# Kernel tuning notes

Hardware: AMD Instinct MI355X
Metric: run time of the kernel (lower is better)

## Reference

```python
import jax, jax.numpy as jnp
import numpy as np

# promonet-derived constants
S = 64        # FARGAN_SUBFRAME_SIZE
NSUB = 4      # FARGAN_SUBFRAMES
HOP = 256     # HOPSIZE = S * NSUB
L = 512       # HOPSIZE * FARGAN_PREVIOUS_FRAMES
F = 193       # acoustic features (192) + pitch period channel
G = 64        # GLOBAL_CHANNELS
CH = F - 1 + G  # conditioning width = 256
B = 64
FRAMES = 100


def setup_inputs() -> dict:
    key = jax.random.key(0)
    ks = jax.random.split(key, 24)

    def w(k, o, i):
        return jax.random.normal(k, (o, i), jnp.float32) / np.sqrt(i).astype(np.float32)

    feat = jax.random.normal(ks[0], (B, F - 1, FRAMES), jnp.float32)
    # last channel is the pitch period (rounded to int inside the model)
    period = jax.random.randint(ks[1], (B, 1, FRAMES), 64, 300).astype(jnp.float32)
    features = jnp.concatenate([feat, period], axis=1)  # (B, F, FRAMES)
    return {
        "features": features,
        "global_features": jax.random.normal(ks[2], (B, G), jnp.float32),
        "previous_samples": 0.1 * jax.random.normal(ks[3], (B, L), jnp.float32),
        # conditioning network (3 bias-free linears, tanh after each)
        "Wc1": w(ks[4], CH, CH),
        "Wc2": w(ks[5], CH, CH),
        "Wc3": w(ks[6], 2 * HOP, CH),
        # framewise conv: linear over [subframe_input(4S+4), prev feat state(2S)]
        "Wfw": w(ks[7], S, 6 * S + 4),
        "Wfw_g": w(ks[8], S, S),
        # three GRU cells (bias-free), torch gate order r,z,n
        "Wih1": w(ks[9], 3 * S, 2 * S), "Whh1": w(ks[10], 3 * S, S),
        "Wih2": w(ks[11], 3 * S, 2 * S), "Whh2": w(ks[12], 3 * S, S),
        "Wih3": w(ks[13], 3 * S, 2 * S), "Whh3": w(ks[14], 3 * S, S),
        # GLU gates
        "Wg1": w(ks[15], S, S), "Wg2": w(ks[16], S, S), "Wg3": w(ks[17], S, S),
        "Wsg": w(ks[18], 2 * S, 2 * S),
        # skip dense + output
        "Wsd": w(ks[19], 2 * S, 5 * S),
        "Wout": w(ks[20], S, 2 * S),
    }


def _glu(x, Wg):
    return x * jax.nn.sigmoid(x @ Wg.T)


def _gru(x, h, Wih, Whh):
    gi = x @ Wih.T
    gh = h @ Whh.T
    ir, iz, inew = jnp.split(gi, 3, axis=-1)
    hr, hz, hnew = jnp.split(gh, 3, axis=-1)
    r = jax.nn.sigmoid(ir + hr)
    z = jax.nn.sigmoid(iz + hz)
    n = jnp.tanh(inew + r * hnew)
    return (1.0 - z) * n + z * h


def reference(features, global_features, previous_samples,
              Wc1, Wc2, Wc3, Wfw, Wfw_g,
              Wih1, Whh1, Wih2, Whh2, Wih3, Whh3,
              Wg1, Wg2, Wg3, Wsg, Wsd, Wout):
    Bn = features.shape[0]
    lb_ar = jnp.arange(S + 4)

    def subframe(feat2s, prev, period, states):
        s1, s2, s3, sfw = states
        prev_sub = prev[:, -S:]
        # data-dependent pitch lookback gather with wrap for short periods
        idx = L - period[:, None] + lb_ar[None, :] - 2
        idx = idx - period[:, None] * (idx >= L)
        lookback = jnp.take_along_axis(prev, idx, axis=1)  # (B, S+4)
        sub_in = jnp.concatenate([feat2s, prev_sub, lookback], axis=1)  # (B, 4S+4)
        fw = _glu(jnp.tanh(jnp.concatenate([sub_in, sfw], axis=1) @ Wfw.T), Wfw_g)
        g1 = _gru(jnp.concatenate([fw, prev_sub], 1), s1, Wih1, Whh1)
        o1 = _glu(g1, Wg1)
        g2 = _gru(jnp.concatenate([o1, prev_sub], 1), s2, Wih2, Whh2)
        o2 = _glu(g2, Wg2)
        g3 = _gru(jnp.concatenate([o2, prev_sub], 1), s3, Wih3, Whh3)
        o3 = _glu(g3, Wg3)
        skip = jnp.concatenate([o1, o2, o3, fw, prev_sub], 1)  # (B, 5S)
        so = _glu(jnp.tanh(skip @ Wsd.T), Wsg)
        out = jnp.tanh(so @ Wout.T)  # (B, S)
        return out, (g1, g2, g3, feat2s)

    def frame_step(carry, feat_t):
        prev, states = carry
        period = jnp.round(feat_t[:, -1]).astype(jnp.int32)
        x = jnp.concatenate([feat_t[:, :-1], global_features], axis=1)
        c = jnp.tanh(jnp.tanh(jnp.tanh(x @ Wc1.T) @ Wc2.T) @ Wc3.T)  # (B, 2*HOP)
        subs = c.reshape(Bn, 2 * S, NSUB)
        outs = []
        for k in range(NSUB):  # fixed tiny unroll over subframes
            out, states = subframe(subs[:, :, k], prev, period, states)
            prev = jnp.concatenate([prev[:, S:], out], axis=1)
            outs.append(out)
        return (prev, states), jnp.concatenate(outs, axis=1)  # (B, HOP)

    dt = features.dtype
    states0 = (jnp.zeros((Bn, S), dt), jnp.zeros((Bn, S), dt),
               jnp.zeros((Bn, S), dt), jnp.zeros((Bn, 2 * S), dt))
    feats_t = jnp.transpose(features, (2, 0, 1))  # (frames, B, F)
    _, sigs = jax.lax.scan(frame_step, (previous_samples, states0), feats_t)
    # (frames, B, HOP) -> (B, 1, frames*HOP)
    return jnp.transpose(sigs, (1, 0, 2)).reshape(Bn, 1, -1)
```

## Files before the change

kernel.cpp:

```cpp
#include <hip/hip_runtime.h>
#include <hip/hip_bf16.h>

#define SS      64
#define NSUB    4
#define LPREV   512
#define NF      193
#define NFRAMES 100
#define BATCH   64
#define RPW     16

typedef __attribute__((ext_vector_type(8))) short   short8;
typedef __attribute__((ext_vector_type(4))) float   floatx4;

__device__ __forceinline__ float bf2f(unsigned short u) {
    return __uint_as_float(((unsigned int)u) << 16);
}
__device__ __forceinline__ unsigned short f2bf(float x) {
    unsigned int u = __float_as_uint(x);
    return (unsigned short)((u + 0x7fffu + ((u >> 16) & 1u)) >> 16);
}
__device__ __forceinline__ unsigned int packbf(float a, float b) {
    return (unsigned int)f2bf(a) | ((unsigned int)f2bf(b) << 16);
}
__device__ __forceinline__ float fexp2(float x) {
#if __has_builtin(__builtin_amdgcn_exp2f)
    return __builtin_amdgcn_exp2f(x);
#else
    return exp2f(x);
#endif
}
__device__ __forceinline__ float frcp(float x) {
#if __has_builtin(__builtin_amdgcn_rcpf)
    return __builtin_amdgcn_rcpf(x);
#else
    return 1.0f / x;
#endif
}
__device__ __forceinline__ float fsig(float x) {
    return frcp(1.0f + fexp2(-1.442695041f * x));
}
__device__ __forceinline__ float ftanh(float x) {
    return fmaf(2.0f, frcp(1.0f + fexp2(-2.885390082f * x)), -1.0f);
}
__device__ __forceinline__ float ld1f(int f32, const void* p, size_t i) {
    if (f32) return ((const float*)p)[i];
    return bf2f(((const unsigned short*)p)[i]);
}
__device__ __forceinline__ float lo16(unsigned int u) { return __uint_as_float(u << 16); }
__device__ __forceinline__ float hi16(unsigned int u) { return __uint_as_float(u & 0xffff0000u); }

__device__ __forceinline__ floatx4 mf(short8 a, short8 b, floatx4 c) {
    return __builtin_amdgcn_mfma_f32_16x16x32_bf16(a, b, c, 0, 0, 0);
}

__device__ __forceinline__ short8 ldA(const unsigned short* buf, int strideU,
                                      int m, int kb, int q) {
    const unsigned int* p = (const unsigned int*)buf + m * strideU + kb * 16 + q * 4;
    uint4 u = *(const uint4*)p;
    return __builtin_bit_cast(short8, u);
}
__device__ __forceinline__ short8 ldB(const uint4* __restrict__ w, int idx) {
    return __builtin_bit_cast(short8, w[idx]);
}

#define OFF_FW   0
#define OFF_FWG  3328
#define OFF_GRU(G) (3840 + 4608*(G))
#define OFF_WG(G)  (17664 + 512*(G))
#define OFF_SD   19200
#define OFF_SG   24320
#define OFF_OUT  26368
#define NFRAG    27392

__global__ void fargan_detect(const void* feats, int* flag) {
    const float* pf = (const float*)feats;
    int ok = 1;
    for (int f = 0; f < 50; ++f) {
        float v = pf[192 * NFRAMES + f];
        if (!(v >= 63.0f && v <= 301.0f)) { ok = 0; break; }
    }
    *flag = ok;
}

__global__ __launch_bounds__(256) void fargan_prep(
    const int* __restrict__ flag,
    const void* Wfw, const void* Wfwg,
    const void* Wih1, const void* Whh1, const void* Wih2, const void* Whh2,
    const void* Wih3, const void* Whh3,
    const void* Wg1, const void* Wg2, const void* Wg3,
    const void* Wsg, const void* Wsd, const void* Wout,
    uint4* __restrict__ wbuf)
{
    int fi = blockIdx.x * 256 + threadIdx.x;
    if (fi >= NFRAG) return;
    int f32 = *flag;
    const void* mats[14] = {Wfw, Wfwg, Wih1, Whh1, Wih2, Whh2, Wih3, Whh3,
                            Wg1, Wg2, Wg3, Wsg, Wsd, Wout};
    const int NSEG = 20;
    const int sb[NSEG]  = {0,3328, 3840,5376,6912,7936, 8448,9984,11520,12544,
                           13056,14592,16128,17152, 17664,18176,18688, 19200,24320,26368};
    const int sa[NSEG]  = {0,1, 2,2,2,3, 4,4,4,5, 6,6,6,7, 8,9,10, 12,11,13};
    const int sbx[NSEG] = {-1,-1, 3,3,-1,-1, 5,5,-1,-1, 7,7,-1,-1, -1,-1,-1, -1,-1,-1};
    const int sro[NSEG] = {0,0, 0,64,128,128, 0,64,128,128, 0,64,128,128, 0,0,0, 0,0,0};
    const int skb[NSEG] = {13,2, 6,6,4,2, 6,6,4,2, 6,6,4,2, 2,2,2, 10,4,4};
    const int ska[NSEG] = {388,64, 128,128,128,64, 128,128,128,64, 128,128,128,64,
                           64,64,64, 320,128,128};
    const int skr[NSEG] = {388,64, 192,192,128,64, 192,192,128,64, 192,192,128,64,
                           64,64,64, 320,128,128};
    int s = 0;
    for (int i = 1; i < NSEG; ++i) if (fi >= sb[i]) s = i;
    int local = fi - sb[s];
    int ln = local & 15, lq = (local >> 4) & 3, tkb = local >> 6;
    int KB = skb[s];
    int kb = tkb % KB, tile = tkb / KB;
    int row = sro[s] + tile * 16 + ln;
    int Ka = ska[s], Kr = skr[s];
    union { unsigned short h[8]; uint4 v; } u;
#pragma unroll
    for (int j = 0; j < 8; ++j) {
        int k = kb * 32 + lq * 8 + j;
        unsigned short val = 0;
        if (k < Kr) {
            const void* m; size_t off;
            if (sbx[s] >= 0 && k >= Ka) { m = mats[sbx[s]]; off = (size_t)row * 64 + (k - Ka); }
            else                        { m = mats[sa[s]];  off = (size_t)row * Ka + k; }
            val = f32 ? f2bf(((const float*)m)[off]) : ((const unsigned short*)m)[off];
        }
        u.h[j] = val;
    }
    wbuf[fi] = u.v;
}

__global__ __launch_bounds__(256) void fargan_prep_conv(
    const int* __restrict__ flag,
    const void* Wc1, const void* Wc2, const void* Wc3,
    unsigned int* __restrict__ wct)
{
    int idx = blockIdx.x * 256 + threadIdx.x;
    if (idx >= 131072) return;
    int f32 = *flag;
    const void* W; int n, k2;
    if (idx < 32768)      { W = Wc1; k2 = idx >> 8, n = idx & 255; }
    else if (idx < 65536) { W = Wc2; k2 = (idx - 32768) >> 8; n = idx & 255; }
    else                  { W = Wc3; k2 = (idx - 65536) >> 9; n = (idx - 65536) & 511; }
    size_t off = (size_t)n * 256 + 2 * k2;
    unsigned int v;
    if (f32) {
        const float* p = (const float*)W + off;
        v = packbf(p[0], p[1]);
    } else {
        v = *(const unsigned int*)((const unsigned short*)W + off);
    }
    wct[idx] = v;
}

template<bool F32>
__device__ __forceinline__ void conv_body(
    const void* __restrict__ feats, const void* __restrict__ gfeat,
    const unsigned int* __restrict__ wct, float* __restrict__ cbuf)
{
    int blk = blockIdx.x;
    int b = blk / NFRAMES, f = blk - b * NFRAMES;
    int t = threadIdx.x;
    __shared__ float xa[256], xb[256];

    float v;
    if (t < 192) v = ld1f(F32 ? 1 : 0, feats, (size_t)b * (NF * NFRAMES) + t * NFRAMES + f);
    else         v = ld1f(F32 ? 1 : 0, gfeat, (size_t)b * 64 + (t - 192));
    xa[t] = v;
    __syncthreads();

    const unsigned int* w1 = wct;
    const unsigned int* w2 = wct + 32768;
    const unsigned int* w3 = wct + 65536;

    float a0 = 0.f, a1 = 0.f;
#pragma unroll 8
    for (int k2 = 0; k2 < 128; ++k2) {
        unsigned int u = w1[k2 * 256 + t];
        a0 = fmaf(lo16(u), xa[2 * k2], a0);
        a1 = fmaf(hi16(u), xa[2 * k2 + 1], a1);
    }
    xb[t] = ftanh(a0 + a1);
    __syncthreads();

    a0 = 0.f; a1 = 0.f;
#pragma unroll 8
    for (int k2 = 0; k2 < 128; ++k2) {
        unsigned int u = w2[k2 * 256 + t];
        a0 = fmaf(lo16(u), xb[2 * k2], a0);
        a1 = fmaf(hi16(u), xb[2 * k2 + 1], a1);
    }
    xa[t] = ftanh(a0 + a1);
    __syncthreads();

    a0 = 0.f; a1 = 0.f;
    float b0 = 0.f, b1 = 0.f;
#pragma unroll 8
    for (int k2 = 0; k2 < 128; ++k2) {
        unsigned int u = w3[k2 * 512 + t];
        unsigned int u2 = w3[k2 * 512 + t + 256];
        a0 = fmaf(lo16(u),  xa[2 * k2],     a0);
        a1 = fmaf(hi16(u),  xa[2 * k2 + 1], a1);
        b0 = fmaf(lo16(u2), xa[2 * k2],     b0);
        b1 = fmaf(hi16(u2), xa[2 * k2 + 1], b1);
    }
    float* co = cbuf + ((size_t)b * NFRAMES + f) * 512;
    int e0 = t, e1 = t + 256;
    co[(e0 & 3) * 128 + (e0 >> 2)] = ftanh(a0 + a1);
    co[(e1 & 3) * 128 + (e1 >> 2)] = ftanh(b0 + b1);
}

__global__ __launch_bounds__(256) void fargan_conv(
    const void* feats, const void* gfeat,
    const int* flag, const unsigned int* wct, float* cbuf)
{
    if (*flag) conv_body<true>(feats, gfeat, wct, cbuf);
    else       conv_body<false>(feats, gfeat, wct, cbuf);
}


__global__ __launch_bounds__(256, 1) void fargan_seq(
    const void* __restrict__ feats, const void* __restrict__ prev_in,
    const int* __restrict__ flag, const float* __restrict__ cbuf,
    const uint4* __restrict__ wbuf, void* __restrict__ outp)
{
    const int t = threadIdx.x;
    const int b0 = blockIdx.x * RPW;
    const int lane = t & 63, w = t >> 6;
    const int lq = lane >> 4, ln = lane & 15;
    const int nj = 16 * w + ln;
    const int f32 = *flag;

    __shared__ __align__(16) unsigned short hist[RPW * 520];
    __shared__ __align__(16) unsigned short catb[RPW * 424];
    __shared__ __align__(16) unsigned short xg  [RPW * 200];
    __shared__ __align__(16) unsigned short skx [RPW * 328];
    __shared__ __align__(16) unsigned short sdbb[RPW * 136];
    __shared__ __align__(16) unsigned short sobb[RPW * 136];
    __shared__ __align__(16) unsigned short vpre[RPW * 72];
    __shared__ __align__(16) unsigned short svp [RPW * 72];
    __shared__ __align__(16) unsigned short wsd[128 * 328];
    __shared__ int period_s[RPW];

    short8 Bfw[13], Bfwg[2], Bout[4];
    short8 Br[3][6], Bz[3][6], Bi[3][4], Bh[3][2], Bg[3][2];
    short8 Bsg[2][4];
#pragma unroll
    for (int kb = 0; kb < 13; ++kb) Bfw[kb] = ldB(wbuf, OFF_FW + (w * 13 + kb) * 64 + lane);
#pragma unroll
    for (int kb = 0; kb < 2; ++kb)  Bfwg[kb] = ldB(wbuf, OFF_FWG + (w * 2 + kb) * 64 + lane);
#pragma unroll
    for (int G = 0; G < 3; ++G) {
        const int OR = OFF_GRU(G), OZ = OR + 1536, OI = OR + 3072, OH = OR + 4096;
#pragma unroll
        for (int kb = 0; kb < 6; ++kb) {
            Br[G][kb] = ldB(wbuf, OR + (w * 6 + kb) * 64 + lane);
            Bz[G][kb] = ldB(wbuf, OZ + (w * 6 + kb) * 64 + lane);
        }
#pragma unroll
        for (int kb = 0; kb < 4; ++kb) Bi[G][kb] = ldB(wbuf, OI + (w * 4 + kb) * 64 + lane);
#pragma unroll
        for (int kb = 0; kb < 2; ++kb) {
            Bh[G][kb] = ldB(wbuf, OH + (w * 2 + kb) * 64 + lane);
            Bg[G][kb] = ldB(wbuf, OFF_WG(G) + (w * 2 + kb) * 64 + lane);
        }
    }
#pragma unroll
    for (int tile = 0; tile < 2; ++tile)
#pragma unroll
        for (int kb = 0; kb < 4; ++kb)
            Bsg[tile][kb] = ldB(wbuf, OFF_SG + ((2 * w + tile) * 4 + kb) * 64 + lane);
#pragma unroll
    for (int kb = 0; kb < 4; ++kb) Bout[kb] = ldB(wbuf, OFF_OUT + (w * 4 + kb) * 64 + lane);

    for (int fi = t; fi < 8 * 10 * 64; fi += 256) {
        int lane2 = fi & 63, tkb = fi >> 6;
        int kb = tkb % 10, tile = tkb / 10;
        int lq2 = lane2 >> 4, ln2 = lane2 & 15;
        int row = tile * 16 + ln2;
        uint4 v = wbuf[OFF_SD + fi];
        *(uint4*)((unsigned int*)wsd + row * 164 + kb * 16 + lq2 * 4) = v;
    }

    for (int i = t; i < RPW * 424; i += 256) catb[i] = 0;
    for (int i = t; i < RPW * 200; i += 256) xg[i] = 0;
    for (int i = t; i < RPW * 328; i += 256) skx[i] = 0;
    for (int i = t; i < RPW * 136; i += 256) { sdbb[i] = 0; sobb[i] = 0; }
    for (int i = t; i < RPW * 72;  i += 256) { vpre[i] = 0; svp[i] = 0; }
    for (int i = t; i < RPW * 512; i += 256) {
        int row = i >> 9, c = i & 511;
        hist[row * 520 + c] = f2bf(ld1f(f32, prev_in, (size_t)(b0 + row) * LPREV + c));
    }
    __syncthreads();
    for (int i = t; i < RPW * 64; i += 256) {
        int row = i >> 6, c = i & 63;
        unsigned short h = hist[row * 520 + 448 + c];
        catb[row * 424 + 128 + c] = h;
        skx [row * 328 + 256 + c] = h;
        xg  [row * 200 + 64  + c] = h;
    }

    floatx4 svr[3];
#pragma unroll
    for (int G = 0; G < 3; ++G) svr[G] = (floatx4){0.f, 0.f, 0.f, 0.f};

    const int prow = t >> 4, px16 = t & 15, pe8 = (t & 15) * 8;
    float pfc[8];
    {
        const float* cr0 = cbuf + ((size_t)(b0 + prow) * NFRAMES + 0) * 512 + 0 * 128 + pe8;
#pragma unroll
        for (int i = 0; i < 8; ++i) pfc[i] = cr0[i];
    }
    float pper = 0.f;
    if (t < RPW)
        pper = ld1f(f32, feats, (size_t)(b0 + t) * (NF * NFRAMES) + (NF - 1) * NFRAMES + 0);
    __syncthreads();

    const floatx4 z4 = {0.f, 0.f, 0.f, 0.f};
    int base = 0;
    for (int f = 0; f < NFRAMES; ++f) {
        if (t < RPW) period_s[t] = (int)rintf(pper);
        __syncthreads();
        if (t < RPW) {
            int fN = (f + 1 < NFRAMES) ? f + 1 : f;
            pper = ld1f(f32, feats, (size_t)(b0 + t) * (NF * NFRAMES) + (NF - 1) * NFRAMES + fN);
        }

        for (int kk = 0; kk < NSUB; ++kk) {
            {
                int row = prow;
                unsigned int* cat32 = (unsigned int*)catb;
                int cb = row * 212;
                int e8 = pe8;
                unsigned int o0 = cat32[cb + (e8 >> 1) + 0];
                unsigned int o1 = cat32[cb + (e8 >> 1) + 1];
                unsigned int o2 = cat32[cb + (e8 >> 1) + 2];
                unsigned int o3 = cat32[cb + (e8 >> 1) + 3];
                cat32[cb + 130 + (e8 >> 1) + 0] = o0;
                cat32[cb + 130 + (e8 >> 1) + 1] = o1;
                cat32[cb + 130 + (e8 >> 1) + 2] = o2;
                cat32[cb + 130 + (e8 >> 1) + 3] = o3;
                cat32[cb + (e8 >> 1) + 0] = packbf(pfc[0], pfc[1]);
                cat32[cb + (e8 >> 1) + 1] = packbf(pfc[2], pfc[3]);
                cat32[cb + (e8 >> 1) + 2] = packbf(pfc[4], pfc[5]);
                cat32[cb + (e8 >> 1) + 3] = packbf(pfc[6], pfc[7]);
                {
                    int sN = f * 4 + kk + 1;
                    if (sN > NFRAMES * 4 - 1) sN = NFRAMES * 4 - 1;
                    int fN = sN >> 2, kN = sN & 3;
                    const float* nc = cbuf + ((size_t)(b0 + row) * NFRAMES + fN) * 512
                                    + kN * 128 + e8;
#pragma unroll
                    for (int i = 0; i < 8; ++i) pfc[i] = nc[i];
                }
                int per = period_s[row];
#pragma unroll
                for (int ii = 0; ii < 5; ++ii) {
                    int i = px16 * 5 + ii;
                    if (i < 68) {
                        int idx = LPREV - per + i - 2;
                        if (idx >= LPREV) idx -= per;
                        catb[row * 424 + 192 + i] = hist[row * 520 + ((base + idx) & 511)];
                    }
                }
            }
            __syncthreads();

            {
                floatx4 C0 = z4, C1 = z4;
#pragma unroll
                for (int kb = 0; kb < 13; ++kb) {
                    short8 a = ldA(catb, 212, ln, kb, lq);
                    if (kb & 1) C1 = mf(a, Bfw[kb], C1);
                    else        C0 = mf(a, Bfw[kb], C0);
                }
#pragma unroll
                for (int r = 0; r < 4; ++r) {
                    int m = 4 * lq + r;
                    vpre[m * 72 + nj] = f2bf(ftanh(C0[r] + C1[r]));
                }
            }
            __syncthreads();

            {
                floatx4 C = z4;
#pragma unroll
                for (int kb = 0; kb < 2; ++kb)
                    C = mf(ldA(vpre, 36, ln, kb, lq), Bfwg[kb], C);
#pragma unroll
                for (int r = 0; r < 4; ++r) {
                    int m = 4 * lq + r;
                    float vp = bf2f(vpre[m * 72 + nj]);
                    unsigned short ob = f2bf(vp * fsig(C[r]));
                    skx[m * 328 + 192 + nj] = ob;
                    xg [m * 200 + nj]       = ob;
                    xg [m * 200 + 128 + nj] = f2bf(svr[0][r]);
                }
            }
            __syncthreads();

#pragma unroll
            for (int G = 0; G < 3; ++G) {
                {
                    floatx4 Cr = z4, Cz = z4, Ci = z4, Ch = z4;
#pragma unroll
                    for (int kb = 0; kb < 6; ++kb) {
                        short8 a = ldA(xg, 100, ln, kb, lq);
                        Cr = mf(a, Br[G][kb], Cr);
                        Cz = mf(a, Bz[G][kb], Cz);
                        if (kb < 4) Ci = mf(a, Bi[G][kb], Ci);
                        else        Ch = mf(a, Bh[G][kb - 4], Ch);
                    }
#pragma unroll
                    for (int r = 0; r < 4; ++r) {
                        int m = 4 * lq + r;
                        float rr = fsig(Cr[r]);
                        float zz = fsig(Cz[r]);
                        float nn = ftanh(Ci[r] + rr * Ch[r]);
                        float sn = fmaf(zz, svr[G][r] - nn, nn);
                        svr[G][r] = sn;
                        svp[m * 72 + nj] = f2bf(sn);
                    }
                }
                __syncthreads();
                {
                    floatx4 C = z4;
#pragma unroll
                    for (int kb = 0; kb < 2; ++kb)
                        C = mf(ldA(svp, 36, ln, kb, lq), Bg[G][kb], C);
#pragma unroll
                    for (int r = 0; r < 4; ++r) {
                        int m = 4 * lq + r;
                        unsigned short ob = f2bf(svr[G][r] * fsig(C[r]));
                        skx[m * 328 + G * 64 + nj] = ob;
                        if (G < 2) {
                            xg[m * 200 + nj]       = ob;
                            xg[m * 200 + 128 + nj] = f2bf(svr[G + 1][r]);
                        }
                    }
                }
                __syncthreads();
            }

            {
                floatx4 C00 = z4, C01 = z4, C10 = z4, C11 = z4;
                int n0 = 32 * w + ln, n1 = n0 + 16;
#pragma unroll
                for (int kb = 0; kb < 10; ++kb) {
                    short8 a   = ldA(skx, 164, ln, kb, lq);
                    short8 b0f = ldA(wsd, 164, n0, kb, lq);
                    short8 b1f = ldA(wsd, 164, n1, kb, lq);
                    if (kb & 1) { C01 = mf(a, b0f, C01); C11 = mf(a, b1f, C11); }
                    else        { C00 = mf(a, b0f, C00); C10 = mf(a, b1f, C10); }
                }
#pragma unroll
                for (int r = 0; r < 4; ++r) {
                    int m = 4 * lq + r;
                    sdbb[m * 136 + n0] = f2bf(ftanh(C00[r] + C01[r]));
                    sdbb[m * 136 + n1] = f2bf(ftanh(C10[r] + C11[r]));
                }
            }
            __syncthreads();

            {
                floatx4 C0 = z4, C1 = z4;
                int n0 = 32 * w + ln, n1 = n0 + 16;
#pragma unroll
                for (int kb = 0; kb < 4; ++kb) {
                    short8 a = ldA(sdbb, 68, ln, kb, lq);
                    C0 = mf(a, Bsg[0][kb], C0);
                    C1 = mf(a, Bsg[1][kb], C1);
                }
#pragma unroll
                for (int r = 0; r < 4; ++r) {
                    int m = 4 * lq + r;
                    float s0 = bf2f(sdbb[m * 136 + n0]);
                    float s1 = bf2f(sdbb[m * 136 + n1]);
                    sobb[m * 136 + n0] = f2bf(s0 * fsig(C0[r]));
                    sobb[m * 136 + n1] = f2bf(s1 * fsig(C1[r]));
                }
            }
            __syncthreads();

            {
                floatx4 C = z4;
#pragma unroll
                for (int kb = 0; kb < 4; ++kb)
                    C = mf(ldA(sobb, 68, ln, kb, lq), Bout[kb], C);
#pragma unroll
                for (int r = 0; r < 4; ++r) {
                    int m = 4 * lq + r;
                    float ov = ftanh(C[r]);
                    unsigned short ob = f2bf(ov);
                    hist[m * 520 + ((base + nj) & 511)] = ob;
                    catb[m * 424 + 128 + nj] = ob;
                    skx [m * 328 + 256 + nj] = ob;
                    xg  [m * 200 + 64  + nj] = ob;
                    size_t oi = (size_t)(b0 + m) * (NFRAMES * NSUB * SS)
                              + f * (NSUB * SS) + kk * SS + nj;
                    if (f32) ((float*)outp)[oi] = ov;
                    else     ((unsigned short*)outp)[oi] = ob;
                }
            }
            __syncthreads();

            base += SS;
        }
    }
}

extern "C" void kernel_launch(void* const* d_in, const int* in_sizes, int n_in,
                              void* d_out, int out_size, void* d_ws, size_t ws_size,
                              hipStream_t stream) {
    const void* feats = d_in[0];
    const void* gfeat = d_in[1];
    const void* prev  = d_in[2];
    const void* Wc1   = d_in[3];
    const void* Wc2   = d_in[4];
    const void* Wc3   = d_in[5];
    const void* Wfw   = d_in[6];
    const void* Wfwg  = d_in[7];
    const void* Wih1  = d_in[8];
    const void* Whh1  = d_in[9];
    const void* Wih2  = d_in[10];
    const void* Whh2  = d_in[11];
    const void* Wih3  = d_in[12];
    const void* Whh3  = d_in[13];
    const void* Wg1   = d_in[14];
    const void* Wg2   = d_in[15];
    const void* Wg3   = d_in[16];
    const void* Wsg   = d_in[17];
    const void* Wsd   = d_in[18];
    const void* Wout  = d_in[19];

    int*          flag = (int*)d_ws;
    float*        cbuf = (float*)((char*)d_ws + 256);
    unsigned int* wct  = (unsigned int*)((char*)d_ws + 256 + 13107200);
    uint4*        wbuf = (uint4*)((char*)d_ws + 256 + 13107200 + 524288);

    fargan_detect<<<1, 1, 0, stream>>>(feats, flag);
    fargan_prep<<<(NFRAG + 255) / 256, 256, 0, stream>>>(flag, Wfw, Wfwg,
        Wih1, Whh1, Wih2, Whh2, Wih3, Whh3, Wg1, Wg2, Wg3, Wsg, Wsd, Wout, wbuf);
    fargan_prep_conv<<<512, 256, 0, stream>>>(flag, Wc1, Wc2, Wc3, wct);
    fargan_conv<<<BATCH * NFRAMES, 256, 0, stream>>>(feats, gfeat, flag, wct, cbuf);
    fargan_seq<<<BATCH / RPW, 256, 0, stream>>>(feats, prev, flag, cbuf, wbuf, d_out);
}
```

Before: 2.618 ms.

## Duplicate MFMA work across two wave groups to halve per-thread epilogue

The sequential kernel now launches 512 threads instead of 256. The extra four waves recompute the same MFMA tiles, and each half handles only two of the four accumulator rows in the transcendental-heavy epilogues (sigmoid, tanh, GRU updates). The shared-memory staging loops are rebalanced across the 512 threads. The aim is to shorten the serial per-subframe critical path, since epilogue math dominates a latency-bound recurrence. The cost is duplicated MFMA and weight-register work plus more waves contending at every barrier.

Measured after the change: 5.849 ms. +123.4%, slower.

```diff
diff --git a/kernel.cpp b/kernel.cpp
--- a/kernel.cpp
+++ b/kernel.cpp
@@ -51,6 +51,13 @@
 
 __device__ __forceinline__ floatx4 mf(short8 a, short8 b, floatx4 c) {
     return __builtin_amdgcn_mfma_f32_16x16x32_bf16(a, b, c, 0, 0, 0);
+}
+
+__device__ __forceinline__ float2 selh(const floatx4 C, int h) {
+    float2 v;
+    if (h) { v.x = C[2]; v.y = C[3]; }
+    else   { v.x = C[0]; v.y = C[1]; }
+    return v;
 }
 
 __device__ __forceinline__ short8 ldA(const unsigned short* buf, int strideU,
@@ -220,16 +227,18 @@
 }
 
 
-__global__ __launch_bounds__(256, 1) void fargan_seq(
+__global__ __launch_bounds__(512, 1) void fargan_seq(
     const void* __restrict__ feats, const void* __restrict__ prev_in,
     const int* __restrict__ flag, const float* __restrict__ cbuf,
     const uint4* __restrict__ wbuf, void* __restrict__ outp)
 {
     const int t = threadIdx.x;
     const int b0 = blockIdx.x * RPW;
-    const int lane = t & 63, w = t >> 6;
+    const int lane = t & 63, w8 = t >> 6;
+    const int w = w8 & 3, h = w8 >> 2;
     const int lq = lane >> 4, ln = lane & 15;
     const int nj = 16 * w + ln;
+    const int m0 = 4 * lq + 2 * h;
     const int f32 = *flag;
 
     __shared__ __align__(16) unsigned short hist[RPW * 520];
@@ -274,7 +283,7 @@
 #pragma unroll
     for (int kb = 0; kb < 4; ++kb) Bout[kb] = ldB(wbuf, OFF_OUT + (w * 4 + kb) * 64 + lane);
 
-    for (int fi = t; fi < 8 * 10 * 64; fi += 256) {
+    for (int fi = t; fi < 8 * 10 * 64; fi += 512) {
         int lane2 = fi & 63, tkb = fi >> 6;
         int kb = tkb % 10, tile = tkb / 10;
         int lq2 = lane2 >> 4, ln2 = lane2 & 15;
@@ -283,34 +292,32 @@
         *(uint4*)((unsigned int*)wsd + row * 164 + kb * 16 + lq2 * 4) = v;
     }
 
-    for (int i = t; i < RPW * 424; i += 256) catb[i] = 0;
-    for (int i = t; i < RPW * 200; i += 256) xg[i] = 0;
-    for (int i = t; i < RPW * 328; i += 256) skx[i] = 0;
-    for (int i = t; i < RPW * 136; i += 256) { sdbb[i] = 0; sobb[i] = 0; }
-    for (int i = t; i < RPW * 72;  i += 256) { vpre[i] = 0; svp[i] = 0; }
-    for (int i = t; i < RPW * 512; i += 256) {
+    for (int i = t; i < RPW * 424; i += 512) catb[i] = 0;
+    for (int i = t; i < RPW * 200; i += 512) xg[i] = 0;
+    for (int i = t; i < RPW * 328; i += 512) skx[i] = 0;
+    for (int i = t; i < RPW * 136; i += 512) { sdbb[i] = 0; sobb[i] = 0; }
+    for (int i = t; i < RPW * 72;  i += 512) { vpre[i] = 0; svp[i] = 0; }
+    for (int i = t; i < RPW * 512; i += 512) {
         int row = i >> 9, c = i & 511;
         hist[row * 520 + c] = f2bf(ld1f(f32, prev_in, (size_t)(b0 + row) * LPREV + c));
     }
     __syncthreads();
-    for (int i = t; i < RPW * 64; i += 256) {
+    for (int i = t; i < RPW * 64; i += 512) {
         int row = i >> 6, c = i & 63;
-        unsigned short h = hist[row * 520 + 448 + c];
-        catb[row * 424 + 128 + c] = h;
-        skx [row * 328 + 256 + c] = h;
-        xg  [row * 200 + 64  + c] = h;
-    }
-
-    floatx4 svr[3];
-#pragma unroll
-    for (int G = 0; G < 3; ++G) svr[G] = (floatx4){0.f, 0.f, 0.f, 0.f};
-
-    const int prow = t >> 4, px16 = t & 15, pe8 = (t & 15) * 8;
-    float pfc[8];
+        unsigned short hh = hist[row * 520 + 448 + c];
+        catb[row * 424 + 128 + c] = hh;
+        skx [row * 328 + 256 + c] = hh;
+        xg  [row * 200 + 64  + c] = hh;
+    }
+
+    float svlo[3] = {0.f, 0.f, 0.f}, svhi[3] = {0.f, 0.f, 0.f};
+
+    const int prow = t >> 5, ps32 = t & 31, pe4 = (t & 31) * 4;
+    float pfc[4];
     {
-        const float* cr0 = cbuf + ((size_t)(b0 + prow) * NFRAMES + 0) * 512 + 0 * 128 + pe8;
-#pragma unroll
-        for (int i = 0; i < 8; ++i) pfc[i] = cr0[i];
+        const float* cr0 = cbuf + ((size_t)(b0 + prow) * NFRAMES + 0) * 512 + pe4;
+#pragma unroll
+        for (int i = 0; i < 4; ++i) pfc[i] = cr0[i];
     }
     float pper = 0.f;
     if (t < RPW)
@@ -332,32 +339,26 @@
                 int row = prow;
                 unsigned int* cat32 = (unsigned int*)catb;
                 int cb = row * 212;
-                int e8 = pe8;
-                unsigned int o0 = cat32[cb + (e8 >> 1) + 0];
-                unsigned int o1 = cat32[cb + (e8 >> 1) + 1];
-                unsigned int o2 = cat32[cb + (e8 >> 1) + 2];
-                unsigned int o3 = cat32[cb + (e8 >> 1) + 3];
-                cat32[cb + 130 + (e8 >> 1) + 0] = o0;
-                cat32[cb + 130 + (e8 >> 1) + 1] = o1;
-                cat32[cb + 130 + (e8 >> 1) + 2] = o2;
-                cat32[cb + 130 + (e8 >> 1) + 3] = o3;
-                cat32[cb + (e8 >> 1) + 0] = packbf(pfc[0], pfc[1]);
-                cat32[cb + (e8 >> 1) + 1] = packbf(pfc[2], pfc[3]);
-                cat32[cb + (e8 >> 1) + 2] = packbf(pfc[4], pfc[5]);
-                cat32[cb + (e8 >> 1) + 3] = packbf(pfc[6], pfc[7]);
+                int u0 = ps32 * 2;
+                unsigned int o0 = cat32[cb + u0 + 0];
+                unsigned int o1 = cat32[cb + u0 + 1];
+                cat32[cb + 130 + u0 + 0] = o0;
+                cat32[cb + 130 + u0 + 1] = o1;
+                cat32[cb + u0 + 0] = packbf(pfc[0], pfc[1]);
+                cat32[cb + u0 + 1] = packbf(pfc[2], pfc[3]);
                 {
                     int sN = f * 4 + kk + 1;
                     if (sN > NFRAMES * 4 - 1) sN = NFRAMES * 4 - 1;
                     int fN = sN >> 2, kN = sN & 3;
                     const float* nc = cbuf + ((size_t)(b0 + row) * NFRAMES + fN) * 512
-                                    + kN * 128 + e8;
-#pragma unroll
-                    for (int i = 0; i < 8; ++i) pfc[i] = nc[i];
+                                    + kN * 128 + pe4;
+#pragma unroll
+                    for (int i = 0; i < 4; ++i) pfc[i] = nc[i];
                 }
                 int per = period_s[row];
 #pragma unroll
-                for (int ii = 0; ii < 5; ++ii) {
-                    int i = px16 * 5 + ii;
+                for (int ii = 0; ii < 3; ++ii) {
+                    int i = ps32 * 3 + ii;
                     if (i < 68) {
                         int idx = LPREV - per + i - 2;
                         if (idx >= LPREV) idx -= per;
@@ -375,11 +376,9 @@
                     if (kb & 1) C1 = mf(a, Bfw[kb], C1);
                     else        C0 = mf(a, Bfw[kb], C0);
                 }
-#pragma unroll
-                for (int r = 0; r < 4; ++r) {
-                    int m = 4 * lq + r;
-                    vpre[m * 72 + nj] = f2bf(ftanh(C0[r] + C1[r]));
-                }
+                float2 ca = selh(C0, h), cb2 = selh(C1, h);
+                vpre[m0 * 72 + nj]       = f2bf(ftanh(ca.x + cb2.x));
+                vpre[(m0 + 1) * 72 + nj] = f2bf(ftanh(ca.y + cb2.y));
             }
             __syncthreads();
 
@@ -388,15 +387,17 @@
 #pragma unroll
                 for (int kb = 0; kb < 2; ++kb)
                     C = mf(ldA(vpre, 36, ln, kb, lq), Bfwg[kb], C);
-#pragma unroll
-                for (int r = 0; r < 4; ++r) {
-                    int m = 4 * lq + r;
-                    float vp = bf2f(vpre[m * 72 + nj]);
-                    unsigned short ob = f2bf(vp * fsig(C[r]));
-                    skx[m * 328 + 192 + nj] = ob;
-                    xg [m * 200 + nj]       = ob;
-                    xg [m * 200 + 128 + nj] = f2bf(svr[0][r]);
-                }
+                float2 c = selh(C, h);
+                float vpa = bf2f(vpre[m0 * 72 + nj]);
+                float vpb = bf2f(vpre[(m0 + 1) * 72 + nj]);
+                unsigned short oa = f2bf(vpa * fsig(c.x));
+                unsigned short ob = f2bf(vpb * fsig(c.y));
+                skx[m0 * 328 + 192 + nj] = oa;
+                skx[(m0 + 1) * 328 + 192 + nj] = ob;
+                xg [m0 * 200 + nj] = oa;
+                xg [(m0 + 1) * 200 + nj] = ob;
+                xg [m0 * 200 + 128 + nj]       = f2bf(svlo[0]);
+                xg [(m0 + 1) * 200 + 128 + nj] = f2bf(svhi[0]);
             }
             __syncthreads();
 
@@ -412,15 +413,21 @@
                         if (kb < 4) Ci = mf(a, Bi[G][kb], Ci);
                         else        Ch = mf(a, Bh[G][kb - 4], Ch);
                     }
-#pragma unroll
-                    for (int r = 0; r < 4; ++r) {
-                        int m = 4 * lq + r;
-                        float rr = fsig(Cr[r]);
-                        float zz = fsig(Cz[r]);
-                        float nn = ftanh(Ci[r] + rr * Ch[r]);
-                        float sn = fmaf(zz, svr[G][r] - nn, nn);
-                        svr[G][r] = sn;
-                        svp[m * 72 + nj] = f2bf(sn);
+                    float2 cr = selh(Cr, h), cz = selh(Cz, h);
+                    float2 ci = selh(Ci, h), ch = selh(Ch, h);
+                    {
+                        float rr = fsig(cr.x), zz = fsig(cz.x);
+                        float nn = ftanh(ci.x + rr * ch.x);
+                        float sn = fmaf(zz, svlo[G] - nn, nn);
+                        svlo[G] = sn;
+                        svp[m0 * 72 + nj] = f2bf(sn);
+                    }
+                    {
+                        float rr = fsig(cr.y), zz = fsig(cz.y);
+                        float nn = ftanh(ci.y + rr * ch.y);
+                        float sn = fmaf(zz, svhi[G] - nn, nn);
+                        svhi[G] = sn;
+                        svp[(m0 + 1) * 72 + nj] = f2bf(sn);
                     }
                 }
                 __syncthreads();
@@ -429,15 +436,16 @@
 #pragma unroll
                     for (int kb = 0; kb < 2; ++kb)
                         C = mf(ldA(svp, 36, ln, kb, lq), Bg[G][kb], C);
-#pragma unroll
-                    for (int r = 0; r < 4; ++r) {
-                        int m = 4 * lq + r;
-                        unsigned short ob = f2bf(svr[G][r] * fsig(C[r]));
-                        skx[m * 328 + G * 64 + nj] = ob;
-                        if (G < 2) {
-                            xg[m * 200 + nj]       = ob;
-                            xg[m * 200 + 128 + nj] = f2bf(svr[G + 1][r]);
-                        }
+                    float2 c = selh(C, h);
+                    unsigned short oa = f2bf(svlo[G] * fsig(c.x));
+                    unsigned short ob = f2bf(svhi[G] * fsig(c.y));
+                    skx[m0 * 328 + G * 64 + nj] = oa;
+                    skx[(m0 + 1) * 328 + G * 64 + nj] = ob;
+                    if (G < 2) {
+                        xg[m0 * 200 + nj] = oa;
+                        xg[(m0 + 1) * 200 + nj] = ob;
+                        xg[m0 * 200 + 128 + nj]       = f2bf(svlo[G + 1]);
+                        xg[(m0 + 1) * 200 + 128 + nj] = f2bf(svhi[G + 1]);
                     }
                 }
                 __syncthreads();
@@ -454,12 +462,12 @@
                     if (kb & 1) { C01 = mf(a, b0f, C01); C11 = mf(a, b1f, C11); }
                     else        { C00 = mf(a, b0f, C00); C10 = mf(a, b1f, C10); }
                 }
-#pragma unroll
-                for (int r = 0; r < 4; ++r) {
-                    int m = 4 * lq + r;
-                    sdbb[m * 136 + n0] = f2bf(ftanh(C00[r] + C01[r]));
-                    sdbb[m * 136 + n1] = f2bf(ftanh(C10[r] + C11[r]));
-                }
+                float2 a0 = selh(C00, h), a1 = selh(C01, h);
+                float2 b0v = selh(C10, h), b1v = selh(C11, h);
+                sdbb[m0 * 136 + n0]       = f2bf(ftanh(a0.x + a1.x));
+                sdbb[(m0 + 1) * 136 + n0] = f2bf(ftanh(a0.y + a1.y));
+                sdbb[m0 * 136 + n1]       = f2bf(ftanh(b0v.x + b1v.x));
+                sdbb[(m0 + 1) * 136 + n1] = f2bf(ftanh(b0v.y + b1v.y));
             }
             __syncthreads();
 
@@ -472,14 +480,15 @@
                     C0 = mf(a, Bsg[0][kb], C0);
                     C1 = mf(a, Bsg[1][kb], C1);
                 }
-#pragma unroll
-                for (int r = 0; r < 4; ++r) {
-                    int m = 4 * lq + r;
-                    float s0 = bf2f(sdbb[m * 136 + n0]);
-                    float s1 = bf2f(sdbb[m * 136 + n1]);
-                    sobb[m * 136 + n0] = f2bf(s0 * fsig(C0[r]));
-                    sobb[m * 136 + n1] = f2bf(s1 * fsig(C1[r]));
-                }
+                float2 c0 = selh(C0, h), c1 = selh(C1, h);
+                float sa0 = bf2f(sdbb[m0 * 136 + n0]);
+                float sa1 = bf2f(sdbb[(m0 + 1) * 136 + n0]);
+                float sb0 = bf2f(sdbb[m0 * 136 + n1]);
+                float sb1 = bf2f(sdbb[(m0 + 1) * 136 + n1]);
+                sobb[m0 * 136 + n0]       = f2bf(sa0 * fsig(c0.x));
+                sobb[(m0 + 1) * 136 + n0] = f2bf(sa1 * fsig(c0.y));
+                sobb[m0 * 136 + n1]       = f2bf(sb0 * fsig(c1.x));
+                sobb[(m0 + 1) * 136 + n1] = f2bf(sb1 * fsig(c1.y));
             }
             __syncthreads();
 
@@ -488,10 +497,11 @@
 #pragma unroll
                 for (int kb = 0; kb < 4; ++kb)
                     C = mf(ldA(sobb, 68, ln, kb, lq), Bout[kb], C);
-#pragma unroll
-                for (int r = 0; r < 4; ++r) {
-                    int m = 4 * lq + r;
-                    float ov = ftanh(C[r]);
+                float2 c = selh(C, h);
+#pragma unroll
+                for (int r2 = 0; r2 < 2; ++r2) {
+                    int m = m0 + r2;
+                    float ov = ftanh(r2 ? c.y : c.x);
                     unsigned short ob = f2bf(ov);
                     hist[m * 520 + ((base + nj) & 511)] = ob;
                     catb[m * 424 + 128 + nj] = ob;
@@ -544,5 +554,5 @@
         Wih1, Whh1, Wih2, Whh2, Wih3, Whh3, Wg1, Wg2, Wg3, Wsg, Wsd, Wout, wbuf);
     fargan_prep_conv<<<512, 256, 0, stream>>>(flag, Wc1, Wc2, Wc3, wct);
     fargan_conv<<<BATCH * NFRAMES, 256, 0, stream>>>(feats, gfeat, flag, wct, cbuf);
-    fargan_seq<<<BATCH / RPW, 256, 0, stream>>>(feats, prev, flag, cbuf, wbuf, d_out);
-}
+    fargan_seq<<<BATCH / RPW, 512, 0, stream>>>(feats, prev, flag, cbuf, wbuf, d_out);
+}
```

## Store conditioning in bf16 and stage per-frame conditioning in LDS

Applied to the files above, without the earlier changes.

The conv kernel now writes the conditioning buffer as bf16 rather than fp32, halving its global footprint. The sequential kernel loads each frame's conditioning with wide vector loads into a shared-memory buffer once per frame, replacing the per-subframe register prefetch from global memory. In bf16 mode the output is written once per frame from the history ring with 16-byte stores instead of scalar per-subframe stores. The trade-offs are an extra barrier per frame, more shared memory, and the loss of the overlapped period prefetch.

Result: slower. 2.680 ms (+2.4%).

```diff
diff --git a/kernel.cpp b/kernel.cpp
--- a/kernel.cpp
+++ b/kernel.cpp
@@ -157,7 +157,7 @@
 template<bool F32>
 __device__ __forceinline__ void conv_body(
     const void* __restrict__ feats, const void* __restrict__ gfeat,
-    const unsigned int* __restrict__ wct, float* __restrict__ cbuf)
+    const unsigned int* __restrict__ wct, unsigned short* __restrict__ cb16)
 {
     int blk = blockIdx.x;
     int b = blk / NFRAMES, f = blk - b * NFRAMES;
@@ -205,24 +205,24 @@
         b0 = fmaf(lo16(u2), xa[2 * k2],     b0);
         b1 = fmaf(hi16(u2), xa[2 * k2 + 1], b1);
     }
-    float* co = cbuf + ((size_t)b * NFRAMES + f) * 512;
+    unsigned short* co = cb16 + ((size_t)b * NFRAMES + f) * 512;
     int e0 = t, e1 = t + 256;
-    co[(e0 & 3) * 128 + (e0 >> 2)] = ftanh(a0 + a1);
-    co[(e1 & 3) * 128 + (e1 >> 2)] = ftanh(b0 + b1);
+    co[(e0 & 3) * 128 + (e0 >> 2)] = f2bf(ftanh(a0 + a1));
+    co[(e1 & 3) * 128 + (e1 >> 2)] = f2bf(ftanh(b0 + b1));
 }
 
 __global__ __launch_bounds__(256) void fargan_conv(
     const void* feats, const void* gfeat,
-    const int* flag, const unsigned int* wct, float* cbuf)
+    const int* flag, const unsigned int* wct, unsigned short* cb16)
 {
-    if (*flag) conv_body<true>(feats, gfeat, wct, cbuf);
-    else       conv_body<false>(feats, gfeat, wct, cbuf);
+    if (*flag) conv_body<true>(feats, gfeat, wct, cb16);
+    else       conv_body<false>(feats, gfeat, wct, cb16);
 }
 
 
 __global__ __launch_bounds__(256, 1) void fargan_seq(
     const void* __restrict__ feats, const void* __restrict__ prev_in,
-    const int* __restrict__ flag, const float* __restrict__ cbuf,
+    const int* __restrict__ flag, const unsigned short* __restrict__ cb16,
     const uint4* __restrict__ wbuf, void* __restrict__ outp)
 {
     const int t = threadIdx.x;
@@ -238,9 +238,9 @@
     __shared__ __align__(16) unsigned short skx [RPW * 328];
     __shared__ __align__(16) unsigned short sdbb[RPW * 136];
     __shared__ __align__(16) unsigned short sobb[RPW * 136];
-    __shared__ __align__(16) unsigned short vpre[RPW * 72];
-    __shared__ __align__(16) unsigned short svp [RPW * 72];
+    __shared__ __align__(16) unsigned short v64 [RPW * 72];
     __shared__ __align__(16) unsigned short wsd[128 * 328];
+    __shared__ __align__(16) unsigned int   cframe[RPW * 260];
     __shared__ int period_s[RPW];
 
     short8 Bfw[13], Bfwg[2], Bout[4];
@@ -287,7 +287,8 @@
     for (int i = t; i < RPW * 200; i += 256) xg[i] = 0;
     for (int i = t; i < RPW * 328; i += 256) skx[i] = 0;
     for (int i = t; i < RPW * 136; i += 256) { sdbb[i] = 0; sobb[i] = 0; }
-    for (int i = t; i < RPW * 72;  i += 256) { vpre[i] = 0; svp[i] = 0; }
+    for (int i = t; i < RPW * 72;  i += 256) v64[i] = 0;
+    for (int i = t; i < RPW * 260; i += 256) cframe[i] = 0;
     for (int i = t; i < RPW * 512; i += 256) {
         int row = i >> 9, c = i & 511;
         hist[row * 520 + c] = f2bf(ld1f(f32, prev_in, (size_t)(b0 + row) * LPREV + c));
@@ -295,69 +296,56 @@
     __syncthreads();
     for (int i = t; i < RPW * 64; i += 256) {
         int row = i >> 6, c = i & 63;
-        unsigned short h = hist[row * 520 + 448 + c];
-        catb[row * 424 + 128 + c] = h;
-        skx [row * 328 + 256 + c] = h;
-        xg  [row * 200 + 64  + c] = h;
+        unsigned short hh = hist[row * 520 + 448 + c];
+        catb[row * 424 + 128 + c] = hh;
+        skx [row * 328 + 256 + c] = hh;
+        xg  [row * 200 + 64  + c] = hh;
     }
 
     floatx4 svr[3];
 #pragma unroll
     for (int G = 0; G < 3; ++G) svr[G] = (floatx4){0.f, 0.f, 0.f, 0.f};
-
-    const int prow = t >> 4, px16 = t & 15, pe8 = (t & 15) * 8;
-    float pfc[8];
-    {
-        const float* cr0 = cbuf + ((size_t)(b0 + prow) * NFRAMES + 0) * 512 + 0 * 128 + pe8;
-#pragma unroll
-        for (int i = 0; i < 8; ++i) pfc[i] = cr0[i];
-    }
-    float pper = 0.f;
-    if (t < RPW)
-        pper = ld1f(f32, feats, (size_t)(b0 + t) * (NF * NFRAMES) + (NF - 1) * NFRAMES + 0);
     __syncthreads();
 
     const floatx4 z4 = {0.f, 0.f, 0.f, 0.f};
     int base = 0;
     for (int f = 0; f < NFRAMES; ++f) {
-        if (t < RPW) period_s[t] = (int)rintf(pper);
+        for (int i = t; i < RPW * 64; i += 256) {
+            int row = i >> 6, j = i & 63;
+            ((unsigned int*)catb)[row * 212 + 130 + j] = cframe[row * 260 + 192 + j];
+        }
         __syncthreads();
-        if (t < RPW) {
-            int fN = (f + 1 < NFRAMES) ? f + 1 : f;
-            pper = ld1f(f32, feats, (size_t)(b0 + t) * (NF * NFRAMES) + (NF - 1) * NFRAMES + fN);
-        }
+        {
+            int row = t >> 4, part = t & 15;
+            const uint4* src = (const uint4*)(cb16 + ((size_t)(b0 + row) * NFRAMES + f) * 512)
+                             + part * 4;
+            uint4* dst = (uint4*)(cframe + row * 260) + part * 4;
+            uint4 s0 = src[0], s1 = src[1], s2 = src[2], s3 = src[3];
+            dst[0] = s0; dst[1] = s1; dst[2] = s2; dst[3] = s3;
+        }
+        if (t < RPW)
+            period_s[t] = (int)rintf(ld1f(f32, feats,
+                (size_t)(b0 + t) * (NF * NFRAMES) + (NF - 1) * NFRAMES + f));
+        __syncthreads();
 
         for (int kk = 0; kk < NSUB; ++kk) {
             {
-                int row = prow;
+                int row = t >> 4, x16 = t & 15;
                 unsigned int* cat32 = (unsigned int*)catb;
                 int cb = row * 212;
-                int e8 = pe8;
-                unsigned int o0 = cat32[cb + (e8 >> 1) + 0];
-                unsigned int o1 = cat32[cb + (e8 >> 1) + 1];
-                unsigned int o2 = cat32[cb + (e8 >> 1) + 2];
-                unsigned int o3 = cat32[cb + (e8 >> 1) + 3];
-                cat32[cb + 130 + (e8 >> 1) + 0] = o0;
-                cat32[cb + 130 + (e8 >> 1) + 1] = o1;
-                cat32[cb + 130 + (e8 >> 1) + 2] = o2;
-                cat32[cb + 130 + (e8 >> 1) + 3] = o3;
-                cat32[cb + (e8 >> 1) + 0] = packbf(pfc[0], pfc[1]);
-                cat32[cb + (e8 >> 1) + 1] = packbf(pfc[2], pfc[3]);
-                cat32[cb + (e8 >> 1) + 2] = packbf(pfc[4], pfc[5]);
-                cat32[cb + (e8 >> 1) + 3] = packbf(pfc[6], pfc[7]);
-                {
-                    int sN = f * 4 + kk + 1;
-                    if (sN > NFRAMES * 4 - 1) sN = NFRAMES * 4 - 1;
-                    int fN = sN >> 2, kN = sN & 3;
-                    const float* nc = cbuf + ((size_t)(b0 + row) * NFRAMES + fN) * 512
-                                    + kN * 128 + e8;
-#pragma unroll
-                    for (int i = 0; i < 8; ++i) pfc[i] = nc[i];
+                const unsigned int* cf = cframe + row * 260;
+                int j4 = x16 * 4;
+#pragma unroll
+                for (int i = 0; i < 4; ++i) cat32[cb + j4 + i] = cf[kk * 64 + j4 + i];
+                if (kk > 0) {
+#pragma unroll
+                    for (int i = 0; i < 4; ++i)
+                        cat32[cb + 130 + j4 + i] = cf[(kk - 1) * 64 + j4 + i];
                 }
                 int per = period_s[row];
 #pragma unroll
                 for (int ii = 0; ii < 5; ++ii) {
-                    int i = px16 * 5 + ii;
+                    int i = x16 * 5 + ii;
                     if (i < 68) {
                         int idx = LPREV - per + i - 2;
                         if (idx >= LPREV) idx -= per;
@@ -378,7 +366,7 @@
 #pragma unroll
                 for (int r = 0; r < 4; ++r) {
                     int m = 4 * lq + r;
-                    vpre[m * 72 + nj] = f2bf(ftanh(C0[r] + C1[r]));
+                    v64[m * 72 + nj] = f2bf(ftanh(C0[r] + C1[r]));
                 }
             }
             __syncthreads();
@@ -387,11 +375,11 @@
                 floatx4 C = z4;
 #pragma unroll
                 for (int kb = 0; kb < 2; ++kb)
-                    C = mf(ldA(vpre, 36, ln, kb, lq), Bfwg[kb], C);
+                    C = mf(ldA(v64, 36, ln, kb, lq), Bfwg[kb], C);
 #pragma unroll
                 for (int r = 0; r < 4; ++r) {
                     int m = 4 * lq + r;
-                    float vp = bf2f(vpre[m * 72 + nj]);
+                    float vp = bf2f(v64[m * 72 + nj]);
                     unsigned short ob = f2bf(vp * fsig(C[r]));
                     skx[m * 328 + 192 + nj] = ob;
                     xg [m * 200 + nj]       = ob;
@@ -420,7 +408,7 @@
                         float nn = ftanh(Ci[r] + rr * Ch[r]);
                         float sn = fmaf(zz, svr[G][r] - nn, nn);
                         svr[G][r] = sn;
-                        svp[m * 72 + nj] = f2bf(sn);
+                        v64[m * 72 + nj] = f2bf(sn);
                     }
                 }
                 __syncthreads();
@@ -428,7 +416,7 @@
                     floatx4 C = z4;
 #pragma unroll
                     for (int kb = 0; kb < 2; ++kb)
-                        C = mf(ldA(svp, 36, ln, kb, lq), Bg[G][kb], C);
+                        C = mf(ldA(v64, 36, ln, kb, lq), Bg[G][kb], C);
 #pragma unroll
                     for (int r = 0; r < 4; ++r) {
                         int m = 4 * lq + r;
@@ -497,15 +485,28 @@
                     catb[m * 424 + 128 + nj] = ob;
                     skx [m * 328 + 256 + nj] = ob;
                     xg  [m * 200 + 64  + nj] = ob;
-                    size_t oi = (size_t)(b0 + m) * (NFRAMES * NSUB * SS)
-                              + f * (NSUB * SS) + kk * SS + nj;
-                    if (f32) ((float*)outp)[oi] = ov;
-                    else     ((unsigned short*)outp)[oi] = ob;
+                    if (f32) {
+                        size_t oi = (size_t)(b0 + m) * (NFRAMES * NSUB * SS)
+                                  + f * (NSUB * SS) + kk * SS + nj;
+                        ((float*)outp)[oi] = ov;
+                    }
                 }
             }
             __syncthreads();
 
             base += SS;
+        }
+
+        if (!f32) {
+            int row = t >> 4, x16 = t & 15;
+            int fb2 = ((f & 1) ? 256 : 0) >> 1;
+            const unsigned int* hsrc = (const unsigned int*)hist + row * 260 + fb2 + x16 * 8;
+            uint4 v0 = *(const uint4*)(hsrc);
+            uint4 v1 = *(const uint4*)(hsrc + 4);
+            unsigned short* op = (unsigned short*)outp
+                + (size_t)(b0 + row) * (NFRAMES * 256) + f * 256 + x16 * 16;
+            *(uint4*)(op)     = v0;
+            *(uint4*)(op + 8) = v1;
         }
     }
 }
@@ -534,15 +535,15 @@
     const void* Wsd   = d_in[18];
     const void* Wout  = d_in[19];
 
-    int*          flag = (int*)d_ws;
-    float*        cbuf = (float*)((char*)d_ws + 256);
-    unsigned int* wct  = (unsigned int*)((char*)d_ws + 256 + 13107200);
-    uint4*        wbuf = (uint4*)((char*)d_ws + 256 + 13107200 + 524288);
+    int*            flag = (int*)d_ws;
+    unsigned short* cb16 = (unsigned short*)((char*)d_ws + 256);
+    unsigned int*   wct  = (unsigned int*)((char*)d_ws + 256 + 6553600);
+    uint4*          wbuf = (uint4*)((char*)d_ws + 256 + 6553600 + 524288);
 
     fargan_detect<<<1, 1, 0, stream>>>(feats, flag);
     fargan_prep<<<(NFRAG + 255) / 256, 256, 0, stream>>>(flag, Wfw, Wfwg,
         Wih1, Whh1, Wih2, Whh2, Wih3, Whh3, Wg1, Wg2, Wg3, Wsg, Wsd, Wout, wbuf);
     fargan_prep_conv<<<512, 256, 0, stream>>>(flag, Wc1, Wc2, Wc3, wct);
-    fargan_conv<<<BATCH * NFRAMES, 256, 0, stream>>>(feats, gfeat, flag, wct, cbuf);
-    fargan_seq<<<BATCH / RPW, 256, 0, stream>>>(feats, prev, flag, cbuf, wbuf, d_out);
-}
+    fargan_conv<<<BATCH * NFRAMES, 256, 0, stream>>>(feats, gfeat, flag, wct, cb16);
+    fargan_seq<<<BATCH / RPW, 256, 0, stream>>>(feats, prev, flag, cb16, wbuf, d_out);
+}
```
